# Optimization experiments

Measured on AMD Instinct MI355X. Metric: run time of the kernel, lower is better.

Reference implementation:

```python
import jax, jax.numpy as jnp
import numpy as np

B = 8192
NV = 778   # MANO vertices
NJ = 16    # LBS joints
PARENTS = np.array([0, 0, 1, 2, 0, 4, 5, 0, 7, 8, 0, 10, 11, 0, 13, 14])


def quat2mat(quat):
    # quat: [N,4] (w,x,y,z) -> [N,3,3]
    q = quat / jnp.linalg.norm(quat, axis=1, keepdims=True)
    w, x, y, z = q[:, 0], q[:, 1], q[:, 2], q[:, 3]
    w2, x2, y2, z2 = w * w, x * x, y * y, z * z
    wx, wy, wz = w * x, w * y, w * z
    xy, xz, yz = x * y, x * z, y * z
    R = jnp.stack([
        w2 + x2 - y2 - z2, 2 * xy - 2 * wz, 2 * wy + 2 * xz,
        2 * wz + 2 * xy, w2 - x2 + y2 - z2, 2 * yz - 2 * wx,
        2 * xz - 2 * wy, 2 * wx + 2 * yz, w2 - x2 - y2 + z2,
    ], axis=1)
    return R.reshape(-1, 3, 3)


def batch_rodrigues(theta):
    # theta: [N,3] axis-angle -> [N,3,3]
    angle = jnp.linalg.norm(theta + 1e-8, axis=1, keepdims=True)
    normalized = theta / angle
    half = angle * 0.5
    quat = jnp.concatenate([jnp.cos(half), jnp.sin(half) * normalized], axis=1)
    return quat2mat(quat)


def qmul(q, r):
    # Hamilton product, (w,x,y,z); q,r: [N,4]
    w1, x1, y1, z1 = q[:, 0], q[:, 1], q[:, 2], q[:, 3]
    w2, x2, y2, z2 = r[:, 0], r[:, 1], r[:, 2], r[:, 3]
    return jnp.stack([
        w1 * w2 - x1 * x2 - y1 * y2 - z1 * z2,
        w1 * x2 + x1 * w2 + y1 * z2 - z1 * y2,
        w1 * y2 - x1 * z2 + y1 * w2 + z1 * x2,
        w1 * z2 + x1 * y2 - y1 * x2 + z1 * w2,
    ], axis=1)


def make_A(R, t):
    # R: [B,J,3,3], t: [B,J,3] -> [B,J,4,4]
    Bn, J = R.shape[0], R.shape[1]
    top = jnp.concatenate([R, t[..., None]], axis=-1)              # [B,J,3,4]
    bot = jnp.broadcast_to(jnp.array([0., 0., 0., 1.], R.dtype), (Bn, J, 1, 4))
    return jnp.concatenate([top, bot], axis=-2)


def mano_forward(theta, delta_quat, user_shape, init_quat, init_trans,
                 v_template, shapedirs, J_regressor, posedirs, weights):
    Bn = theta.shape[0]
    beta = jnp.broadcast_to(user_shape, (Bn, user_shape.shape[-1]))
    v_shaped = (beta @ shapedirs).reshape(Bn, NV, 3) + v_template   # [B,778,3]
    J = jnp.einsum('bvc,vj->bjc', v_shaped, J_regressor)            # [B,21,3]

    Rs = batch_rodrigues(theta.reshape(-1, 3)).reshape(Bn, 15, 3, 3)
    pose_feature = (Rs - jnp.eye(3, dtype=Rs.dtype)).reshape(Bn, 135)
    v_posed = (pose_feature @ posedirs).reshape(Bn, NV, 3) + v_shaped

    quat = qmul(delta_quat, jnp.broadcast_to(init_quat, (Bn, 4)))
    root_R = quat2mat(quat)                                          # [B,3,3]
    Rs_all = jnp.concatenate([root_R[:, None], Rs], axis=1)          # [B,16,3,3]

    Jk = J[:, :NJ]                                                   # [B,16,3]
    rel = Jk - Jk[:, PARENTS]
    rel = rel.at[:, 0].set(Jk[:, 0])                                 # root keeps absolute pos
    A_local = make_A(Rs_all, rel)                                    # [B,16,4,4]

    # kinematic chain (fixed 16-joint tree)
    results = [A_local[:, 0]]
    for i in range(1, NJ):
        results.append(results[PARENTS[i]] @ A_local[:, i])
    G = jnp.stack(results, axis=1)                                   # [B,16,4,4]

    Jw0 = jnp.concatenate([Jk, jnp.zeros((Bn, NJ, 1), Jk.dtype)], axis=-1)
    init_bone = jnp.einsum('bjkl,bjl->bjk', G, Jw0)                  # [B,16,4]
    A = jnp.concatenate([G[..., :3], G[..., 3:] - init_bone[..., None]], axis=-1)

    T = jnp.einsum('vj,bjkl->bvkl', weights, A)                      # [B,778,4,4]
    vp_homo = jnp.concatenate([v_posed, jnp.ones((Bn, NV, 1), v_posed.dtype)], axis=-1)
    verts = jnp.einsum('bvkl,bvl->bvk', T, vp_homo)[..., :3]         # [B,778,3]

    joints = jnp.einsum('bvc,vj->bjc', verts, J_regressor)           # [B,21,3]
    trans = init_trans.reshape(Bn, 1, 3)
    return joints + trans  # get_skin=False path


def setup_inputs() -> dict:
    key = jax.random.key(0)
    ks = jax.random.split(key, 10)
    return {
        'theta': jax.random.normal(ks[0], (B, 45), jnp.float32) * 0.3,
        'delta_quat': jax.random.normal(ks[1], (B, 4), jnp.float32),
        'user_shape': jax.random.normal(ks[2], (1, 10), jnp.float32),
        'init_quat': jax.random.normal(ks[3], (1, 4), jnp.float32),
        'init_trans': jax.random.normal(ks[4], (B, 3), jnp.float32),
        'v_template': jax.random.normal(ks[5], (NV, 3), jnp.float32),
        'shapedirs': jax.random.normal(ks[6], (10, NV * 3), jnp.float32) * 0.01,
        'J_regressor': jax.random.uniform(ks[7], (NV, 21), jnp.float32) / NV,
        'posedirs': jax.random.normal(ks[8], (135, NV * 3), jnp.float32) * 0.01,
        'weights': jax.random.uniform(ks[9], (NV, NJ), jnp.float32),
    }


def reference(theta, delta_quat, user_shape, init_quat, init_trans,
              v_template, shapedirs, J_regressor, posedirs, weights):
    return mano_forward(theta, delta_quat, user_shape, init_quat, init_trans,
                        v_template, shapedirs, J_regressor, posedirs, weights)
```

## Files before the change

kernel.cpp:

```cpp
#include <hip/hip_runtime.h>
#include <math.h>

#define B_SIZE 8192
#define NVERT 778
#define NP 135
#define NEC 416
#define KS16 16

#define OFF_JK    0
#define OFF_C1    64
#define OFF_C0    400
#define OFF_P2    1408
#define OFF_PFT   137488
#define OFF_AT    1243408
#define OFF_PP    137488
#define WS_END    2816272

__device__ inline void quat2mat_dev(float qw, float qx, float qy, float qz, float* R) {
  float n = sqrtf(qw*qw + qx*qx + qy*qy + qz*qz);
  float w = qw/n, x = qx/n, y = qy/n, z = qz/n;
  float w2=w*w, x2=x*x, y2=y*y, z2=z*z;
  float wx=w*x, wy=w*y, wz=w*z, xy=x*y, xz=x*z, yz=y*z;
  R[0]=w2+x2-y2-z2; R[1]=2.f*xy-2.f*wz; R[2]=2.f*wy+2.f*xz;
  R[3]=2.f*wz+2.f*xy; R[4]=w2-x2+y2-z2; R[5]=2.f*yz-2.f*wx;
  R[6]=2.f*xz-2.f*wy; R[7]=2.f*wx+2.f*yz; R[8]=w2-x2-y2+z2;
}

__device__ inline void rodrigues_dev(float tx, float ty, float tz, float* R) {
  float ax = tx + 1e-8f, ay = ty + 1e-8f, az = tz + 1e-8f;
  float angle = sqrtf(ax*ax + ay*ay + az*az);
  float nx = tx/angle, ny = ty/angle, nz = tz/angle;
  float half = 0.5f*angle;
  float cw = cosf(half), sw = sinf(half);
  quat2mat_dev(cw, sw*nx, sw*ny, sw*nz, R);
}

__global__ __launch_bounds__(256) void kA(const float* __restrict__ J_regressor,
                                          const float* __restrict__ weights,
                                          const float* __restrict__ posedirs,
                                          const float* __restrict__ user_shape,
                                          const float* __restrict__ v_template,
                                          const float* __restrict__ shapedirs,
                                          float* __restrict__ ws) {
  int tid = threadIdx.x;
  int bid = blockIdx.x;

  if (bid >= 416) {
    int j = bid - 416;
    __shared__ float red[3*256];
    __shared__ float ush[10];
    if (tid < 10) ush[tid] = user_shape[tid];
    __syncthreads();
    float p0 = 0.f, p1 = 0.f, p2 = 0.f;
    for (int v = tid; v < NVERT; v += 256) {
      float jr = J_regressor[v*21 + j];
      #pragma unroll
      for (int c = 0; c < 3; ++c) {
        int e = 3*v + c;
        float t = v_template[e];
        #pragma unroll
        for (int s = 0; s < 10; ++s) t += ush[s]*shapedirs[s*2334 + e];
        float val = jr * t;
        if (c == 0) p0 += val; else if (c == 1) p1 += val; else p2 += val;
      }
    }
    red[0*256+tid] = p0; red[1*256+tid] = p1; red[2*256+tid] = p2;
    __syncthreads();
    for (int s = 128; s > 0; s >>= 1) {
      if (tid < s) {
        red[0*256+tid] += red[0*256+tid+s];
        red[1*256+tid] += red[1*256+tid+s];
        red[2*256+tid] += red[2*256+tid+s];
      }
      __syncthreads();
    }
    if (tid < 3) ws[OFF_JK + j*3 + tid] = red[tid*256];
    return;
  }

  __shared__ float sJR[49*21];
  __shared__ float sW [49*16];
  __shared__ float sB [64*16];
  __shared__ float ush[10];
  if (tid < 10) ush[tid] = user_shape[tid];
  int ng = bid % 26;
  int ks = bid / 26;
  int vbeg = ks*49;
  int kt = min(NVERT - vbeg, 49);
  __syncthreads();
  for (int idx = tid; idx < kt*21; idx += 256) sJR[idx] = J_regressor[vbeg*21 + idx];
  for (int idx = tid; idx < kt*16; idx += 256) sW[idx]  = weights[vbeg*16 + idx];
  for (int idx = tid; idx < 16*64; idx += 256) {
    int s = idx >> 6, iv = idx & 63;
    if (iv < kt) {
      int ec = ng*16 + s;
      float val;
      if (ec > 408) val = 0.f;
      else if (ec == 408) val = 1.f;
      else {
        int c = ec / 136, pp = ec - c*136;
        int e = 3*(vbeg+iv) + c;
        if (pp == 135) {
          float t = v_template[e];
          #pragma unroll
          for (int s0 = 0; s0 < 10; ++s0) t += ush[s0]*shapedirs[s0*2334 + e];
          val = t;
        } else {
          val = posedirs[pp*2334 + e];
        }
      }
      sB[iv*16 + s] = val;
    }
  }
  __syncthreads();
  if (tid < 168) {
    int cg2 = (tid < 84) ? 0 : 1;
    int r4  = (tid < 84) ? tid : tid - 84;
    int q2 = 4*r4;
    int j2 = q2 >> 4;
    int jb = q2 & 15;
    float acc[4][8];
    #pragma unroll
    for (int r = 0; r < 4; ++r)
      #pragma unroll
      for (int s = 0; s < 8; ++s) acc[r][s] = 0.f;
    for (int i = 0; i < kt; ++i) {
      float jr = sJR[i*21 + j2];
      float4 w4 = *(const float4*)&sW[i*16 + jb];
      float4 b0 = *(const float4*)&sB[i*16 + cg2*8];
      float4 b1 = *(const float4*)&sB[i*16 + cg2*8 + 4];
      float wv[4] = {w4.x, w4.y, w4.z, w4.w};
      #pragma unroll
      for (int r = 0; r < 4; ++r) {
        float s2 = jr * wv[r];
        acc[r][0] += s2*b0.x; acc[r][1] += s2*b0.y;
        acc[r][2] += s2*b0.z; acc[r][3] += s2*b0.w;
        acc[r][4] += s2*b1.x; acc[r][5] += s2*b1.y;
        acc[r][6] += s2*b1.z; acc[r][7] += s2*b1.w;
      }
    }
    float* Pp = ws + OFF_PP + (size_t)ks*NEC*336;
    #pragma unroll
    for (int s = 0; s < 8; ++s) {
      int ec = ng*16 + cg2*8 + s;
      float4 v4 = make_float4(acc[0][s], acc[1][s], acc[2][s], acc[3][s]);
      *(float4*)&Pp[ec*336 + q2] = v4;
    }
  }
}

__global__ void kR(float* __restrict__ ws) {
  int idx = blockIdx.x*256 + threadIdx.x;
  if (idx >= 416*84) return;
  int ec = idx / 84, q4 = idx - ec*84;
  const float* Pp = ws + OFF_PP;
  float4 s = make_float4(0.f, 0.f, 0.f, 0.f);
  #pragma unroll
  for (int ks = 0; ks < KS16; ++ks) {
    float4 v = *(const float4*)&Pp[(size_t)ks*NEC*336 + ec*336 + 4*q4];
    s.x += v.x; s.y += v.y; s.z += v.z; s.w += v.w;
  }
  float sv[4] = {s.x, s.y, s.z, s.w};
  #pragma unroll
  for (int r = 0; r < 4; ++r) {
    int q2 = 4*q4 + r;
    int jj2 = q2 >> 4, jj = q2 & 15;
    if (ec < 408) {
      int c = ec / 136, pp = ec - c*136;
      if (pp < 135) ws[OFF_P2 + (size_t)(jj2*135 + pp)*48 + jj*3 + c] = sv[r];
      else          ws[OFF_C0 + jj2*48 + jj*3 + c] = sv[r];
    } else if (ec == 408) {
      ws[OFF_C1 + jj2*16 + jj] = sv[r];
    }
  }
}

__global__ __launch_bounds__(256) void k4_pose(const float* __restrict__ theta,
                                               const float* __restrict__ delta_quat,
                                               const float* __restrict__ init_quat,
                                               float* __restrict__ ws) {
  int bid = blockIdx.x;
  int u  = bid % 6;
  int bb = bid / 6;
  int b  = bb*256 + threadIdx.x;
  __shared__ float jk[48], rel[48];
  if (threadIdx.x < 48) {
    float v = ws[OFF_JK + threadIdx.x];
    jk[threadIdx.x] = v;
    int j = threadIdx.x/3, c = threadIdx.x - j*3;
    float r;
    if (j == 0) r = v;
    else {
      int par = (((j-1) % 3) == 0) ? 0 : (j-1);
      r = v - ws[OFF_JK + par*3 + c];
    }
    rel[threadIdx.x] = r;
  }
  __syncthreads();
  float* pfT = ws + OFF_PFT;
  float* AT  = ws + OFF_AT;

  float w1=delta_quat[b*4+0], x1=delta_quat[b*4+1], y1=delta_quat[b*4+2], z1=delta_quat[b*4+3];
  float w2=init_quat[0], x2=init_quat[1], y2=init_quat[2], z2=init_quat[3];
  float qw = w1*w2 - x1*x2 - y1*y2 - z1*z2;
  float qx = w1*x2 + x1*w2 + y1*z2 - z1*y2;
  float qy = w1*y2 - x1*z2 + y1*w2 + z1*x2;
  float qz = w1*z2 + x1*y2 - y1*x2 + z1*w2;
  float G[12];
  quat2mat_dev(qw, qx, qy, qz, G);
  G[9] = rel[0]; G[10] = rel[1]; G[11] = rel[2];

  if (u == 5) {
    #pragma unroll
    for (int c = 0; c < 3; ++c) {
      float g0 = G[c*3+0], g1 = G[c*3+1], g2 = G[c*3+2];
      AT[(size_t)(c*4+0)*B_SIZE + b] = g0;
      AT[(size_t)(c*4+1)*B_SIZE + b] = g1;
      AT[(size_t)(c*4+2)*B_SIZE + b] = g2;
      AT[(size_t)(c*4+3)*B_SIZE + b] = G[9+c] - (g0*jk[0] + g1*jk[1] + g2*jk[2]);
    }
    return;
  }

  #pragma unroll
  for (int mstep = 0; mstep < 3; ++mstep) {
    int j = 3*u + 1 + mstep;
    int i = j - 1;
    float R[9];
    rodrigues_dev(theta[b*45+3*i+0], theta[b*45+3*i+1], theta[b*45+3*i+2], R);
    pfT[(size_t)(9*i+0)*B_SIZE + b] = R[0]-1.f;
    pfT[(size_t)(9*i+1)*B_SIZE + b] = R[1];
    pfT[(size_t)(9*i+2)*B_SIZE + b] = R[2];
    pfT[(size_t)(9*i+3)*B_SIZE + b] = R[3];
    pfT[(size_t)(9*i+4)*B_SIZE + b] = R[4]-1.f;
    pfT[(size_t)(9*i+5)*B_SIZE + b] = R[5];
    pfT[(size_t)(9*i+6)*B_SIZE + b] = R[6];
    pfT[(size_t)(9*i+7)*B_SIZE + b] = R[7];
    pfT[(size_t)(9*i+8)*B_SIZE + b] = R[8]-1.f;
    float nG[12];
    const float* rj = rel + j*3;
    #pragma unroll
    for (int r3 = 0; r3 < 3; ++r3) {
      float a0 = G[r3*3+0], a1 = G[r3*3+1], a2 = G[r3*3+2];
      nG[r3*3+0] = a0*R[0] + a1*R[3] + a2*R[6];
      nG[r3*3+1] = a0*R[1] + a1*R[4] + a2*R[7];
      nG[r3*3+2] = a0*R[2] + a1*R[5] + a2*R[8];
      nG[9+r3]   = G[9+r3] + a0*rj[0] + a1*rj[1] + a2*rj[2];
    }
    #pragma unroll
    for (int k = 0; k < 12; ++k) G[k] = nG[k];
    const float* jkj = jk + j*3;
    #pragma unroll
    for (int c = 0; c < 3; ++c) {
      float g0 = G[c*3+0], g1 = G[c*3+1], g2 = G[c*3+2];
      AT[(size_t)(j*12 + c*4+0)*B_SIZE + b] = g0;
      AT[(size_t)(j*12 + c*4+1)*B_SIZE + b] = g1;
      AT[(size_t)(j*12 + c*4+2)*B_SIZE + b] = g2;
      AT[(size_t)(j*12 + c*4+3)*B_SIZE + b] = G[9+c] - (g0*jkj[0] + g1*jkj[1] + g2*jkj[2]);
    }
  }
}

__global__ __launch_bounds__(256) void k5_main(const float* __restrict__ init_trans,
                                               const float* __restrict__ ws,
                                               float* __restrict__ out) {
  int g = blockIdx.x;
  int xcd = g & 7, k = g >> 3;
  int br  = ((k & 3) << 3) | xcd;
  int j2  = k >> 2;
  int b   = br*256 + threadIdx.x;

  float4 acc[12];
  const float4* c04 = (const float4*)(ws + OFF_C0 + j2*48);
  #pragma unroll
  for (int i = 0; i < 12; ++i) acc[i] = c04[i];

  const float* pfT = ws + OFF_PFT;
  const float4* P24 = (const float4*)(ws + OFF_P2);
  #pragma unroll 3
  for (int p = 0; p < NP; ++p) {
    float pf = pfT[(size_t)p*B_SIZE + b];
    const float4* Pr = P24 + (size_t)(j2*135 + p)*12;
    #pragma unroll
    for (int i = 0; i < 12; ++i) {
      float4 pv = Pr[i];
      acc[i].x += pf*pv.x; acc[i].y += pf*pv.y;
      acc[i].z += pf*pv.z; acc[i].w += pf*pv.w;
    }
  }

  float m[48];
  #pragma unroll
  for (int i = 0; i < 12; ++i) {
    m[4*i+0] = acc[i].x; m[4*i+1] = acc[i].y;
    m[4*i+2] = acc[i].z; m[4*i+3] = acc[i].w;
  }

  const float* AT  = ws + OFF_AT;
  const float* c1p = ws + OFF_C1 + j2*16;
  float o0 = 0.f, o1 = 0.f, o2 = 0.f;
  #pragma unroll
  for (int j = 0; j < 16; ++j) {
    float c1 = c1p[j];
    float m0 = m[3*j+0], m1 = m[3*j+1], m2 = m[3*j+2];
    #pragma unroll
    for (int k2 = 0; k2 < 3; ++k2) {
      float a0 = AT[(size_t)(j*12 + k2*4+0)*B_SIZE + b];
      float a1 = AT[(size_t)(j*12 + k2*4+1)*B_SIZE + b];
      float a2 = AT[(size_t)(j*12 + k2*4+2)*B_SIZE + b];
      float a3 = AT[(size_t)(j*12 + k2*4+3)*B_SIZE + b];
      float r = a0*m0 + a1*m1 + a2*m2 + a3*c1;
      if (k2 == 0) o0 += r; else if (k2 == 1) o1 += r; else o2 += r;
    }
  }
  size_t ob = ((size_t)b*21 + j2)*3;
  out[ob+0] = o0 + init_trans[b*3+0];
  out[ob+1] = o1 + init_trans[b*3+1];
  out[ob+2] = o2 + init_trans[b*3+2];
}

extern "C" void kernel_launch(void* const* d_in, const int* in_sizes, int n_in,
                              void* d_out, int out_size, void* d_ws, size_t ws_size,
                              hipStream_t stream) {
  const float* theta       = (const float*)d_in[0];
  const float* delta_quat  = (const float*)d_in[1];
  const float* user_shape  = (const float*)d_in[2];
  const float* init_quat   = (const float*)d_in[3];
  const float* init_trans  = (const float*)d_in[4];
  const float* v_template  = (const float*)d_in[5];
  const float* shapedirs   = (const float*)d_in[6];
  const float* J_regressor = (const float*)d_in[7];
  const float* posedirs    = (const float*)d_in[8];
  const float* weights     = (const float*)d_in[9];
  float* out = (float*)d_out;
  float* ws  = (float*)d_ws;

  kA<<<432, 256, 0, stream>>>(J_regressor, weights, posedirs,
                              user_shape, v_template, shapedirs, ws);
  kR<<<137, 256, 0, stream>>>(ws);
  k4_pose<<<192, 256, 0, stream>>>(theta, delta_quat, init_quat, ws);
  k5_main<<<672, 256, 0, stream>>>(init_trans, ws, out);
}
```

Before: 142.9 us.

## Merge reduce and pose kernels, split k5 pose-blendshape loop across two waves

Moves the partial-sum buffer to a non-overlapping workspace region so the reduction and pose kernels can run as one launch, removing one launch and its serialization. A fallback path keeps the old three-kernel sequence when the workspace is too small. k5_main now uses 512 threads per block: each half handles half of the 135 pose features, and the two partial accumulators are combined through shared memory. This doubles the parallelism of the posedirs GEMV at the cost of about 49 KB of LDS per block, which can limit occupancy. Pose blocks are also remapped so consecutive blocks fall on different XCDs.

Measured after the change: 193.2 us. +35.2%, slower.

```diff
diff --git a/kernel.cpp b/kernel.cpp
--- a/kernel.cpp
+++ b/kernel.cpp
@@ -13,8 +13,9 @@
 #define OFF_P2    1408
 #define OFF_PFT   137488
 #define OFF_AT    1243408
-#define OFF_PP    137488
-#define WS_END    2816272
+#define WS_BASE   2816272
+#define OFF_PP_OVER 137488
+#define OFF_PP_SAFE 2816272
 
 __device__ inline void quat2mat_dev(float qw, float qx, float qy, float qz, float* R) {
   float n = sqrtf(qw*qw + qx*qx + qy*qy + qz*qz);
@@ -35,13 +36,106 @@
   quat2mat_dev(cw, sw*nx, sw*ny, sw*nz, R);
 }
 
+__device__ inline void pose_unit(const float* __restrict__ theta,
+                                 const float* __restrict__ delta_quat,
+                                 const float* __restrict__ init_quat,
+                                 float* __restrict__ ws,
+                                 const float* jk, const float* rel,
+                                 int bb, int u, int lane) {
+  int b = bb*256 + lane;
+  float* pfT = ws + OFF_PFT;
+  float* AT  = ws + OFF_AT;
+  float w1=delta_quat[b*4+0], x1=delta_quat[b*4+1], y1=delta_quat[b*4+2], z1=delta_quat[b*4+3];
+  float w2=init_quat[0], x2=init_quat[1], y2=init_quat[2], z2=init_quat[3];
+  float qw = w1*w2 - x1*x2 - y1*y2 - z1*z2;
+  float qx = w1*x2 + x1*w2 + y1*z2 - z1*y2;
+  float qy = w1*y2 - x1*z2 + y1*w2 + z1*x2;
+  float qz = w1*z2 + x1*y2 - y1*x2 + z1*w2;
+  float G[12];
+  quat2mat_dev(qw, qx, qy, qz, G);
+  G[9] = rel[0]; G[10] = rel[1]; G[11] = rel[2];
+  if (u == 5) {
+    #pragma unroll
+    for (int c = 0; c < 3; ++c) {
+      float g0 = G[c*3+0], g1 = G[c*3+1], g2 = G[c*3+2];
+      AT[(size_t)(c*4+0)*B_SIZE + b] = g0;
+      AT[(size_t)(c*4+1)*B_SIZE + b] = g1;
+      AT[(size_t)(c*4+2)*B_SIZE + b] = g2;
+      AT[(size_t)(c*4+3)*B_SIZE + b] = G[9+c] - (g0*jk[0] + g1*jk[1] + g2*jk[2]);
+    }
+    return;
+  }
+  #pragma unroll
+  for (int mstep = 0; mstep < 3; ++mstep) {
+    int j = 3*u + 1 + mstep;
+    int i = j - 1;
+    float R[9];
+    rodrigues_dev(theta[b*45+3*i+0], theta[b*45+3*i+1], theta[b*45+3*i+2], R);
+    pfT[(size_t)(9*i+0)*B_SIZE + b] = R[0]-1.f;
+    pfT[(size_t)(9*i+1)*B_SIZE + b] = R[1];
+    pfT[(size_t)(9*i+2)*B_SIZE + b] = R[2];
+    pfT[(size_t)(9*i+3)*B_SIZE + b] = R[3];
+    pfT[(size_t)(9*i+4)*B_SIZE + b] = R[4]-1.f;
+    pfT[(size_t)(9*i+5)*B_SIZE + b] = R[5];
+    pfT[(size_t)(9*i+6)*B_SIZE + b] = R[6];
+    pfT[(size_t)(9*i+7)*B_SIZE + b] = R[7];
+    pfT[(size_t)(9*i+8)*B_SIZE + b] = R[8]-1.f;
+    float nG[12];
+    const float* rj = rel + j*3;
+    #pragma unroll
+    for (int r3 = 0; r3 < 3; ++r3) {
+      float a0 = G[r3*3+0], a1 = G[r3*3+1], a2 = G[r3*3+2];
+      nG[r3*3+0] = a0*R[0] + a1*R[3] + a2*R[6];
+      nG[r3*3+1] = a0*R[1] + a1*R[4] + a2*R[7];
+      nG[r3*3+2] = a0*R[2] + a1*R[5] + a2*R[8];
+      nG[9+r3]   = G[9+r3] + a0*rj[0] + a1*rj[1] + a2*rj[2];
+    }
+    #pragma unroll
+    for (int k = 0; k < 12; ++k) G[k] = nG[k];
+    const float* jkj = jk + j*3;
+    #pragma unroll
+    for (int c = 0; c < 3; ++c) {
+      float g0 = G[c*3+0], g1 = G[c*3+1], g2 = G[c*3+2];
+      AT[(size_t)(j*12 + c*4+0)*B_SIZE + b] = g0;
+      AT[(size_t)(j*12 + c*4+1)*B_SIZE + b] = g1;
+      AT[(size_t)(j*12 + c*4+2)*B_SIZE + b] = g2;
+      AT[(size_t)(j*12 + c*4+3)*B_SIZE + b] = G[9+c] - (g0*jkj[0] + g1*jkj[1] + g2*jkj[2]);
+    }
+  }
+}
+
+__device__ inline void kr_task(float* __restrict__ ws, int pp_off, int idx) {
+  if (idx >= 416*84) return;
+  int ec = idx / 84, q4 = idx - ec*84;
+  const float* Pp = ws + pp_off;
+  float4 s = make_float4(0.f, 0.f, 0.f, 0.f);
+  #pragma unroll
+  for (int ks = 0; ks < KS16; ++ks) {
+    float4 v = *(const float4*)&Pp[(size_t)ks*NEC*336 + ec*336 + 4*q4];
+    s.x += v.x; s.y += v.y; s.z += v.z; s.w += v.w;
+  }
+  float sv[4] = {s.x, s.y, s.z, s.w};
+  #pragma unroll
+  for (int r = 0; r < 4; ++r) {
+    int q2 = 4*q4 + r;
+    int jj2 = q2 >> 4, jj = q2 & 15;
+    if (ec < 408) {
+      int c = ec / 136, pp = ec - c*136;
+      if (pp < 135) ws[OFF_P2 + (size_t)(jj2*135 + pp)*48 + jj*3 + c] = sv[r];
+      else          ws[OFF_C0 + jj2*48 + jj*3 + c] = sv[r];
+    } else if (ec == 408) {
+      ws[OFF_C1 + jj2*16 + jj] = sv[r];
+    }
+  }
+}
+
 __global__ __launch_bounds__(256) void kA(const float* __restrict__ J_regressor,
                                           const float* __restrict__ weights,
                                           const float* __restrict__ posedirs,
                                           const float* __restrict__ user_shape,
                                           const float* __restrict__ v_template,
                                           const float* __restrict__ shapedirs,
-                                          float* __restrict__ ws) {
+                                          float* __restrict__ ws, int pp_off) {
   int tid = threadIdx.x;
   int bid = blockIdx.x;
 
@@ -139,7 +233,7 @@
         acc[r][6] += s2*b1.z; acc[r][7] += s2*b1.w;
       }
     }
-    float* Pp = ws + OFF_PP + (size_t)ks*NEC*336;
+    float* Pp = ws + pp_off + (size_t)ks*NEC*336;
     #pragma unroll
     for (int s = 0; s < 8; ++s) {
       int ec = ng*16 + cg2*8 + s;
@@ -149,138 +243,100 @@
   }
 }
 
-__global__ void kR(float* __restrict__ ws) {
-  int idx = blockIdx.x*256 + threadIdx.x;
-  if (idx >= 416*84) return;
-  int ec = idx / 84, q4 = idx - ec*84;
-  const float* Pp = ws + OFF_PP;
-  float4 s = make_float4(0.f, 0.f, 0.f, 0.f);
-  #pragma unroll
-  for (int ks = 0; ks < KS16; ++ks) {
-    float4 v = *(const float4*)&Pp[(size_t)ks*NEC*336 + ec*336 + 4*q4];
-    s.x += v.x; s.y += v.y; s.z += v.z; s.w += v.w;
-  }
-  float sv[4] = {s.x, s.y, s.z, s.w};
-  #pragma unroll
-  for (int r = 0; r < 4; ++r) {
-    int q2 = 4*q4 + r;
-    int jj2 = q2 >> 4, jj = q2 & 15;
-    if (ec < 408) {
-      int c = ec / 136, pp = ec - c*136;
-      if (pp < 135) ws[OFF_P2 + (size_t)(jj2*135 + pp)*48 + jj*3 + c] = sv[r];
-      else          ws[OFF_C0 + jj2*48 + jj*3 + c] = sv[r];
-    } else if (ec == 408) {
-      ws[OFF_C1 + jj2*16 + jj] = sv[r];
-    }
-  }
-}
-
-__global__ __launch_bounds__(256) void k4_pose(const float* __restrict__ theta,
-                                               const float* __restrict__ delta_quat,
-                                               const float* __restrict__ init_quat,
-                                               float* __restrict__ ws) {
+__global__ __launch_bounds__(256) void kRk4(const float* __restrict__ theta,
+                                            const float* __restrict__ delta_quat,
+                                            const float* __restrict__ init_quat,
+                                            float* __restrict__ ws, int pp_off) {
   int bid = blockIdx.x;
-  int u  = bid % 6;
-  int bb = bid / 6;
-  int b  = bb*256 + threadIdx.x;
+  int tid = threadIdx.x;
+  if (bid < 137) {
+    kr_task(ws, pp_off, bid*256 + tid);
+    return;
+  }
   __shared__ float jk[48], rel[48];
-  if (threadIdx.x < 48) {
-    float v = ws[OFF_JK + threadIdx.x];
-    jk[threadIdx.x] = v;
-    int j = threadIdx.x/3, c = threadIdx.x - j*3;
+  if (tid < 48) {
+    float v = ws[OFF_JK + tid];
+    jk[tid] = v;
+    int j = tid/3, c = tid - j*3;
     float r;
     if (j == 0) r = v;
     else {
       int par = (((j-1) % 3) == 0) ? 0 : (j-1);
       r = v - ws[OFF_JK + par*3 + c];
     }
-    rel[threadIdx.x] = r;
+    rel[tid] = r;
   }
   __syncthreads();
-  float* pfT = ws + OFF_PFT;
-  float* AT  = ws + OFF_AT;
-
-  float w1=delta_quat[b*4+0], x1=delta_quat[b*4+1], y1=delta_quat[b*4+2], z1=delta_quat[b*4+3];
-  float w2=init_quat[0], x2=init_quat[1], y2=init_quat[2], z2=init_quat[3];
-  float qw = w1*w2 - x1*x2 - y1*y2 - z1*z2;
-  float qx = w1*x2 + x1*w2 + y1*z2 - z1*y2;
-  float qy = w1*y2 - x1*z2 + y1*w2 + z1*x2;
-  float qz = w1*z2 + x1*y2 - y1*x2 + z1*w2;
-  float G[12];
-  quat2mat_dev(qw, qx, qy, qz, G);
-  G[9] = rel[0]; G[10] = rel[1]; G[11] = rel[2];
-
-  if (u == 5) {
-    #pragma unroll
-    for (int c = 0; c < 3; ++c) {
-      float g0 = G[c*3+0], g1 = G[c*3+1], g2 = G[c*3+2];
-      AT[(size_t)(c*4+0)*B_SIZE + b] = g0;
-      AT[(size_t)(c*4+1)*B_SIZE + b] = g1;
-      AT[(size_t)(c*4+2)*B_SIZE + b] = g2;
-      AT[(size_t)(c*4+3)*B_SIZE + b] = G[9+c] - (g0*jk[0] + g1*jk[1] + g2*jk[2]);
-    }
-    return;
-  }
-
-  #pragma unroll
-  for (int mstep = 0; mstep < 3; ++mstep) {
-    int j = 3*u + 1 + mstep;
-    int i = j - 1;
-    float R[9];
-    rodrigues_dev(theta[b*45+3*i+0], theta[b*45+3*i+1], theta[b*45+3*i+2], R);
-    pfT[(size_t)(9*i+0)*B_SIZE + b] = R[0]-1.f;
-    pfT[(size_t)(9*i+1)*B_SIZE + b] = R[1];
-    pfT[(size_t)(9*i+2)*B_SIZE + b] = R[2];
-    pfT[(size_t)(9*i+3)*B_SIZE + b] = R[3];
-    pfT[(size_t)(9*i+4)*B_SIZE + b] = R[4]-1.f;
-    pfT[(size_t)(9*i+5)*B_SIZE + b] = R[5];
-    pfT[(size_t)(9*i+6)*B_SIZE + b] = R[6];
-    pfT[(size_t)(9*i+7)*B_SIZE + b] = R[7];
-    pfT[(size_t)(9*i+8)*B_SIZE + b] = R[8]-1.f;
-    float nG[12];
-    const float* rj = rel + j*3;
-    #pragma unroll
-    for (int r3 = 0; r3 < 3; ++r3) {
-      float a0 = G[r3*3+0], a1 = G[r3*3+1], a2 = G[r3*3+2];
-      nG[r3*3+0] = a0*R[0] + a1*R[3] + a2*R[6];
-      nG[r3*3+1] = a0*R[1] + a1*R[4] + a2*R[7];
-      nG[r3*3+2] = a0*R[2] + a1*R[5] + a2*R[8];
-      nG[9+r3]   = G[9+r3] + a0*rj[0] + a1*rj[1] + a2*rj[2];
-    }
-    #pragma unroll
-    for (int k = 0; k < 12; ++k) G[k] = nG[k];
-    const float* jkj = jk + j*3;
-    #pragma unroll
-    for (int c = 0; c < 3; ++c) {
-      float g0 = G[c*3+0], g1 = G[c*3+1], g2 = G[c*3+2];
-      AT[(size_t)(j*12 + c*4+0)*B_SIZE + b] = g0;
-      AT[(size_t)(j*12 + c*4+1)*B_SIZE + b] = g1;
-      AT[(size_t)(j*12 + c*4+2)*B_SIZE + b] = g2;
-      AT[(size_t)(j*12 + c*4+3)*B_SIZE + b] = G[9+c] - (g0*jkj[0] + g1*jkj[1] + g2*jkj[2]);
-    }
-  }
-}
-
-__global__ __launch_bounds__(256) void k5_main(const float* __restrict__ init_trans,
+  int s = bid & 7;
+  int t = (bid - 137) >> 3;
+  int bb = s + 8*(t & 3);
+  int u  = t >> 2;
+  pose_unit(theta, delta_quat, init_quat, ws, jk, rel, bb, u, tid);
+}
+
+__global__ void kR_fb(float* __restrict__ ws, int pp_off) {
+  kr_task(ws, pp_off, blockIdx.x*256 + threadIdx.x);
+}
+
+__global__ __launch_bounds__(256) void k4_fb(const float* __restrict__ theta,
+                                             const float* __restrict__ delta_quat,
+                                             const float* __restrict__ init_quat,
+                                             float* __restrict__ ws) {
+  int bid = blockIdx.x;
+  int tid = threadIdx.x;
+  __shared__ float jk[48], rel[48];
+  if (tid < 48) {
+    float v = ws[OFF_JK + tid];
+    jk[tid] = v;
+    int j = tid/3, c = tid - j*3;
+    float r;
+    if (j == 0) r = v;
+    else {
+      int par = (((j-1) % 3) == 0) ? 0 : (j-1);
+      r = v - ws[OFF_JK + par*3 + c];
+    }
+    rel[tid] = r;
+  }
+  __syncthreads();
+  int s = bid & 7;
+  int t = bid >> 3;
+  int bb = s + 8*(t & 3);
+  int u  = t >> 2;
+  pose_unit(theta, delta_quat, init_quat, ws, jk, rel, bb, u, tid);
+}
+
+__global__ __launch_bounds__(512) void k5_main(const float* __restrict__ init_trans,
                                                const float* __restrict__ ws,
                                                float* __restrict__ out) {
+  __shared__ float sM[256*49];
   int g = blockIdx.x;
   int xcd = g & 7, k = g >> 3;
   int br  = ((k & 3) << 3) | xcd;
   int j2  = k >> 2;
-  int b   = br*256 + threadIdx.x;
+  int tid = threadIdx.x;
+  int bl  = tid & 255;
+  int ph  = tid >> 8;
+  int b   = br*256 + bl;
+
+  int pbeg = __builtin_amdgcn_readfirstlane(ph ? 68 : 0);
+  int pend = __builtin_amdgcn_readfirstlane(ph ? NP : 68);
 
   float4 acc[12];
-  const float4* c04 = (const float4*)(ws + OFF_C0 + j2*48);
-  #pragma unroll
-  for (int i = 0; i < 12; ++i) acc[i] = c04[i];
+  if (ph == 0) {
+    const float4* c04 = (const float4*)(ws + OFF_C0 + j2*48);
+    #pragma unroll
+    for (int i = 0; i < 12; ++i) acc[i] = c04[i];
+  } else {
+    #pragma unroll
+    for (int i = 0; i < 12; ++i) acc[i] = make_float4(0.f, 0.f, 0.f, 0.f);
+  }
 
   const float* pfT = ws + OFF_PFT;
-  const float4* P24 = (const float4*)(ws + OFF_P2);
+  const float4* P24 = (const float4*)(ws + OFF_P2) + (size_t)j2*1620;
   #pragma unroll 3
-  for (int p = 0; p < NP; ++p) {
+  for (int p = pbeg; p < pend; ++p) {
     float pf = pfT[(size_t)p*B_SIZE + b];
-    const float4* Pr = P24 + (size_t)(j2*135 + p)*12;
+    const float4* Pr = P24 + p*12;
     #pragma unroll
     for (int i = 0; i < 12; ++i) {
       float4 pv = Pr[i];
@@ -289,34 +345,47 @@
     }
   }
 
-  float m[48];
-  #pragma unroll
-  for (int i = 0; i < 12; ++i) {
-    m[4*i+0] = acc[i].x; m[4*i+1] = acc[i].y;
-    m[4*i+2] = acc[i].z; m[4*i+3] = acc[i].w;
-  }
-
-  const float* AT  = ws + OFF_AT;
-  const float* c1p = ws + OFF_C1 + j2*16;
-  float o0 = 0.f, o1 = 0.f, o2 = 0.f;
-  #pragma unroll
-  for (int j = 0; j < 16; ++j) {
-    float c1 = c1p[j];
-    float m0 = m[3*j+0], m1 = m[3*j+1], m2 = m[3*j+2];
-    #pragma unroll
-    for (int k2 = 0; k2 < 3; ++k2) {
-      float a0 = AT[(size_t)(j*12 + k2*4+0)*B_SIZE + b];
-      float a1 = AT[(size_t)(j*12 + k2*4+1)*B_SIZE + b];
-      float a2 = AT[(size_t)(j*12 + k2*4+2)*B_SIZE + b];
-      float a3 = AT[(size_t)(j*12 + k2*4+3)*B_SIZE + b];
-      float r = a0*m0 + a1*m1 + a2*m2 + a3*c1;
-      if (k2 == 0) o0 += r; else if (k2 == 1) o1 += r; else o2 += r;
-    }
-  }
-  size_t ob = ((size_t)b*21 + j2)*3;
-  out[ob+0] = o0 + init_trans[b*3+0];
-  out[ob+1] = o1 + init_trans[b*3+1];
-  out[ob+2] = o2 + init_trans[b*3+2];
+  if (ph == 1) {
+    float* dst = sM + bl*49;
+    #pragma unroll
+    for (int i = 0; i < 12; ++i) {
+      dst[4*i+0] = acc[i].x; dst[4*i+1] = acc[i].y;
+      dst[4*i+2] = acc[i].z; dst[4*i+3] = acc[i].w;
+    }
+  }
+  __syncthreads();
+  if (ph == 0) {
+    const float* src = sM + bl*49;
+    float m[48];
+    #pragma unroll
+    for (int i = 0; i < 12; ++i) {
+      m[4*i+0] = acc[i].x + src[4*i+0];
+      m[4*i+1] = acc[i].y + src[4*i+1];
+      m[4*i+2] = acc[i].z + src[4*i+2];
+      m[4*i+3] = acc[i].w + src[4*i+3];
+    }
+    const float* AT  = ws + OFF_AT;
+    const float* c1p = ws + OFF_C1 + j2*16;
+    float o0 = 0.f, o1 = 0.f, o2 = 0.f;
+    #pragma unroll
+    for (int j = 0; j < 16; ++j) {
+      float c1 = c1p[j];
+      float m0 = m[3*j+0], m1 = m[3*j+1], m2 = m[3*j+2];
+      #pragma unroll
+      for (int k2 = 0; k2 < 3; ++k2) {
+        float a0 = AT[(size_t)(j*12 + k2*4+0)*B_SIZE + b];
+        float a1 = AT[(size_t)(j*12 + k2*4+1)*B_SIZE + b];
+        float a2 = AT[(size_t)(j*12 + k2*4+2)*B_SIZE + b];
+        float a3 = AT[(size_t)(j*12 + k2*4+3)*B_SIZE + b];
+        float r = a0*m0 + a1*m1 + a2*m2 + a3*c1;
+        if (k2 == 0) o0 += r; else if (k2 == 1) o1 += r; else o2 += r;
+      }
+    }
+    size_t ob = ((size_t)b*21 + j2)*3;
+    out[ob+0] = o0 + init_trans[b*3+0];
+    out[ob+1] = o1 + init_trans[b*3+1];
+    out[ob+2] = o2 + init_trans[b*3+2];
+  }
 }
 
 extern "C" void kernel_launch(void* const* d_in, const int* in_sizes, int n_in,
@@ -335,9 +404,16 @@
   float* out = (float*)d_out;
   float* ws  = (float*)d_ws;
 
-  kA<<<432, 256, 0, stream>>>(J_regressor, weights, posedirs,
-                              user_shape, v_template, shapedirs, ws);
-  kR<<<137, 256, 0, stream>>>(ws);
-  k4_pose<<<192, 256, 0, stream>>>(theta, delta_quat, init_quat, ws);
-  k5_main<<<672, 256, 0, stream>>>(init_trans, ws, out);
-}
+  size_t need = ((size_t)OFF_PP_SAFE + (size_t)KS16*NEC*336) * 4;
+  if (ws_size >= need) {
+    kA<<<432, 256, 0, stream>>>(J_regressor, weights, posedirs,
+                                user_shape, v_template, shapedirs, ws, OFF_PP_SAFE);
+    kRk4<<<329, 256, 0, stream>>>(theta, delta_quat, init_quat, ws, OFF_PP_SAFE);
+  } else {
+    kA<<<432, 256, 0, stream>>>(J_regressor, weights, posedirs,
+                                user_shape, v_template, shapedirs, ws, OFF_PP_OVER);
+    kR_fb<<<137, 256, 0, stream>>>(ws, OFF_PP_OVER);
+    k4_fb<<<192, 256, 0, stream>>>(theta, delta_quat, init_quat, ws);
+  }
+  k5_main<<<672, 512, 0, stream>>>(init_trans, ws, out);
+}
```

## Fuse precompute, reduction and pose kernels into a single prep kernel

Applied to the files above, without the earlier changes.

Replaces the three preparatory kernels (split-K weight contraction, partial-sum reduction, pose chain) with one kernel. The weight contraction now runs one block per output row over the full vertex range, so the split-K partial buffer and the separate reduction pass are gone. The pose blocks each recompute the joint locations locally with a wave-shuffle reduction instead of reading them from a prior kernel. This removes two launches and the workspace round trip, at the cost of redundant joint-regression work in every pose block and less parallel, scalar-FMA contraction per block.

Measured after the change: 183.8 us. 1.29x slower.

```diff
diff --git a/kernel.cpp b/kernel.cpp
--- a/kernel.cpp
+++ b/kernel.cpp
@@ -4,8 +4,6 @@
 #define B_SIZE 8192
 #define NVERT 778
 #define NP 135
-#define NEC 416
-#define KS16 16
 
 #define OFF_JK    0
 #define OFF_C1    64
@@ -13,7 +11,6 @@
 #define OFF_P2    1408
 #define OFF_PFT   137488
 #define OFF_AT    1243408
-#define OFF_PP    137488
 #define WS_END    2816272
 
 __device__ inline void quat2mat_dev(float qw, float qx, float qy, float qz, float* R) {
@@ -35,171 +32,15 @@
   quat2mat_dev(cw, sw*nx, sw*ny, sw*nz, R);
 }
 
-__global__ __launch_bounds__(256) void kA(const float* __restrict__ J_regressor,
-                                          const float* __restrict__ weights,
-                                          const float* __restrict__ posedirs,
-                                          const float* __restrict__ user_shape,
-                                          const float* __restrict__ v_template,
-                                          const float* __restrict__ shapedirs,
-                                          float* __restrict__ ws) {
-  int tid = threadIdx.x;
-  int bid = blockIdx.x;
-
-  if (bid >= 416) {
-    int j = bid - 416;
-    __shared__ float red[3*256];
-    __shared__ float ush[10];
-    if (tid < 10) ush[tid] = user_shape[tid];
-    __syncthreads();
-    float p0 = 0.f, p1 = 0.f, p2 = 0.f;
-    for (int v = tid; v < NVERT; v += 256) {
-      float jr = J_regressor[v*21 + j];
-      #pragma unroll
-      for (int c = 0; c < 3; ++c) {
-        int e = 3*v + c;
-        float t = v_template[e];
-        #pragma unroll
-        for (int s = 0; s < 10; ++s) t += ush[s]*shapedirs[s*2334 + e];
-        float val = jr * t;
-        if (c == 0) p0 += val; else if (c == 1) p1 += val; else p2 += val;
-      }
-    }
-    red[0*256+tid] = p0; red[1*256+tid] = p1; red[2*256+tid] = p2;
-    __syncthreads();
-    for (int s = 128; s > 0; s >>= 1) {
-      if (tid < s) {
-        red[0*256+tid] += red[0*256+tid+s];
-        red[1*256+tid] += red[1*256+tid+s];
-        red[2*256+tid] += red[2*256+tid+s];
-      }
-      __syncthreads();
-    }
-    if (tid < 3) ws[OFF_JK + j*3 + tid] = red[tid*256];
-    return;
-  }
-
-  __shared__ float sJR[49*21];
-  __shared__ float sW [49*16];
-  __shared__ float sB [64*16];
-  __shared__ float ush[10];
-  if (tid < 10) ush[tid] = user_shape[tid];
-  int ng = bid % 26;
-  int ks = bid / 26;
-  int vbeg = ks*49;
-  int kt = min(NVERT - vbeg, 49);
-  __syncthreads();
-  for (int idx = tid; idx < kt*21; idx += 256) sJR[idx] = J_regressor[vbeg*21 + idx];
-  for (int idx = tid; idx < kt*16; idx += 256) sW[idx]  = weights[vbeg*16 + idx];
-  for (int idx = tid; idx < 16*64; idx += 256) {
-    int s = idx >> 6, iv = idx & 63;
-    if (iv < kt) {
-      int ec = ng*16 + s;
-      float val;
-      if (ec > 408) val = 0.f;
-      else if (ec == 408) val = 1.f;
-      else {
-        int c = ec / 136, pp = ec - c*136;
-        int e = 3*(vbeg+iv) + c;
-        if (pp == 135) {
-          float t = v_template[e];
-          #pragma unroll
-          for (int s0 = 0; s0 < 10; ++s0) t += ush[s0]*shapedirs[s0*2334 + e];
-          val = t;
-        } else {
-          val = posedirs[pp*2334 + e];
-        }
-      }
-      sB[iv*16 + s] = val;
-    }
-  }
-  __syncthreads();
-  if (tid < 168) {
-    int cg2 = (tid < 84) ? 0 : 1;
-    int r4  = (tid < 84) ? tid : tid - 84;
-    int q2 = 4*r4;
-    int j2 = q2 >> 4;
-    int jb = q2 & 15;
-    float acc[4][8];
-    #pragma unroll
-    for (int r = 0; r < 4; ++r)
-      #pragma unroll
-      for (int s = 0; s < 8; ++s) acc[r][s] = 0.f;
-    for (int i = 0; i < kt; ++i) {
-      float jr = sJR[i*21 + j2];
-      float4 w4 = *(const float4*)&sW[i*16 + jb];
-      float4 b0 = *(const float4*)&sB[i*16 + cg2*8];
-      float4 b1 = *(const float4*)&sB[i*16 + cg2*8 + 4];
-      float wv[4] = {w4.x, w4.y, w4.z, w4.w};
-      #pragma unroll
-      for (int r = 0; r < 4; ++r) {
-        float s2 = jr * wv[r];
-        acc[r][0] += s2*b0.x; acc[r][1] += s2*b0.y;
-        acc[r][2] += s2*b0.z; acc[r][3] += s2*b0.w;
-        acc[r][4] += s2*b1.x; acc[r][5] += s2*b1.y;
-        acc[r][6] += s2*b1.z; acc[r][7] += s2*b1.w;
-      }
-    }
-    float* Pp = ws + OFF_PP + (size_t)ks*NEC*336;
-    #pragma unroll
-    for (int s = 0; s < 8; ++s) {
-      int ec = ng*16 + cg2*8 + s;
-      float4 v4 = make_float4(acc[0][s], acc[1][s], acc[2][s], acc[3][s]);
-      *(float4*)&Pp[ec*336 + q2] = v4;
-    }
-  }
-}
-
-__global__ void kR(float* __restrict__ ws) {
-  int idx = blockIdx.x*256 + threadIdx.x;
-  if (idx >= 416*84) return;
-  int ec = idx / 84, q4 = idx - ec*84;
-  const float* Pp = ws + OFF_PP;
-  float4 s = make_float4(0.f, 0.f, 0.f, 0.f);
-  #pragma unroll
-  for (int ks = 0; ks < KS16; ++ks) {
-    float4 v = *(const float4*)&Pp[(size_t)ks*NEC*336 + ec*336 + 4*q4];
-    s.x += v.x; s.y += v.y; s.z += v.z; s.w += v.w;
-  }
-  float sv[4] = {s.x, s.y, s.z, s.w};
-  #pragma unroll
-  for (int r = 0; r < 4; ++r) {
-    int q2 = 4*q4 + r;
-    int jj2 = q2 >> 4, jj = q2 & 15;
-    if (ec < 408) {
-      int c = ec / 136, pp = ec - c*136;
-      if (pp < 135) ws[OFF_P2 + (size_t)(jj2*135 + pp)*48 + jj*3 + c] = sv[r];
-      else          ws[OFF_C0 + jj2*48 + jj*3 + c] = sv[r];
-    } else if (ec == 408) {
-      ws[OFF_C1 + jj2*16 + jj] = sv[r];
-    }
-  }
-}
-
-__global__ __launch_bounds__(256) void k4_pose(const float* __restrict__ theta,
-                                               const float* __restrict__ delta_quat,
-                                               const float* __restrict__ init_quat,
-                                               float* __restrict__ ws) {
-  int bid = blockIdx.x;
-  int u  = bid % 6;
-  int bb = bid / 6;
-  int b  = bb*256 + threadIdx.x;
-  __shared__ float jk[48], rel[48];
-  if (threadIdx.x < 48) {
-    float v = ws[OFF_JK + threadIdx.x];
-    jk[threadIdx.x] = v;
-    int j = threadIdx.x/3, c = threadIdx.x - j*3;
-    float r;
-    if (j == 0) r = v;
-    else {
-      int par = (((j-1) % 3) == 0) ? 0 : (j-1);
-      r = v - ws[OFF_JK + par*3 + c];
-    }
-    rel[threadIdx.x] = r;
-  }
-  __syncthreads();
+__device__ inline void pose_unit(const float* __restrict__ theta,
+                                 const float* __restrict__ delta_quat,
+                                 const float* __restrict__ init_quat,
+                                 float* __restrict__ ws,
+                                 const float* jk, const float* rel,
+                                 int bb, int u, int lane) {
+  int b = bb*256 + lane;
   float* pfT = ws + OFF_PFT;
   float* AT  = ws + OFF_AT;
-
   float w1=delta_quat[b*4+0], x1=delta_quat[b*4+1], y1=delta_quat[b*4+2], z1=delta_quat[b*4+3];
   float w2=init_quat[0], x2=init_quat[1], y2=init_quat[2], z2=init_quat[3];
   float qw = w1*w2 - x1*x2 - y1*y2 - z1*z2;
@@ -209,7 +50,6 @@
   float G[12];
   quat2mat_dev(qw, qx, qy, qz, G);
   G[9] = rel[0]; G[10] = rel[1]; G[11] = rel[2];
-
   if (u == 5) {
     #pragma unroll
     for (int c = 0; c < 3; ++c) {
@@ -221,7 +61,6 @@
     }
     return;
   }
-
   #pragma unroll
   for (int mstep = 0; mstep < 3; ++mstep) {
     int j = 3*u + 1 + mstep;
@@ -261,6 +100,137 @@
   }
 }
 
+__global__ __launch_bounds__(384) void kPrep(const float* __restrict__ theta,
+                                             const float* __restrict__ delta_quat,
+                                             const float* __restrict__ init_quat,
+                                             const float* __restrict__ v_template,
+                                             const float* __restrict__ user_shape,
+                                             const float* __restrict__ shapedirs,
+                                             const float* __restrict__ J_regressor,
+                                             const float* __restrict__ posedirs,
+                                             const float* __restrict__ weights,
+                                             float* __restrict__ ws) {
+  __shared__ float smem[4928];
+  int tid = threadIdx.x;
+  int bid = blockIdx.x;
+
+  if (bid < 409) {
+    float* sJR = smem;
+    float* sW  = smem + 2688;
+    float* sB  = smem + 4736;
+    float* ush = smem + 4864;
+    if (tid < 10) ush[tid] = user_shape[tid];
+    int ec = bid;
+    int cc = ec / 136, pp = ec - cc*136;
+    int q2 = tid;
+    int j2 = q2 >> 4, jj = q2 & 15;
+    float acc = 0.f;
+    for (int v0 = 0; v0 < NVERT; v0 += 128) {
+      int kt = min(128, NVERT - v0);
+      __syncthreads();
+      for (int i = tid; i < kt*21; i += 384) sJR[i] = J_regressor[v0*21 + i];
+      for (int i = tid; i < kt*16; i += 384) sW[i]  = weights[v0*16 + i];
+      for (int i = tid; i < kt; i += 384) {
+        float val;
+        if (ec == 408) val = 1.f;
+        else {
+          int e = 3*(v0+i) + cc;
+          if (pp == 135) {
+            float t = v_template[e];
+            #pragma unroll
+            for (int s = 0; s < 10; ++s) t += ush[s]*shapedirs[s*2334 + e];
+            val = t;
+          } else {
+            val = posedirs[pp*2334 + e];
+          }
+        }
+        sB[i] = val;
+      }
+      __syncthreads();
+      if (tid < 336) {
+        for (int i = 0; i < kt; ++i) {
+          float bv = sB[i];
+          acc += sJR[i*21 + j2] * sW[i*16 + jj] * bv;
+        }
+      }
+    }
+    if (tid < 336) {
+      if (ec == 408) {
+        ws[OFF_C1 + j2*16 + jj] = acc;
+      } else if (pp == 135) {
+        ws[OFF_C0 + j2*48 + jj*3 + cc] = acc;
+      } else {
+        ws[OFF_P2 + (size_t)(j2*135 + pp)*48 + jj*3 + cc] = acc;
+      }
+    }
+    return;
+  }
+
+  float* redw = smem;
+  float* jk   = smem + 288;
+  float* rel  = smem + 336;
+  float* ush  = smem + 384;
+  if (tid < 10) ush[tid] = user_shape[tid];
+  __syncthreads();
+  float part[48];
+  #pragma unroll
+  for (int k = 0; k < 48; ++k) part[k] = 0.f;
+  for (int v = tid; v < NVERT; v += 384) {
+    float vs[3];
+    #pragma unroll
+    for (int c = 0; c < 3; ++c) {
+      int e = 3*v + c;
+      float t = v_template[e];
+      #pragma unroll
+      for (int s = 0; s < 10; ++s) t += ush[s]*shapedirs[s*2334 + e];
+      vs[c] = t;
+    }
+    #pragma unroll
+    for (int j = 0; j < 16; ++j) {
+      float jr = J_regressor[v*21 + j];
+      part[j*3+0] += jr*vs[0];
+      part[j*3+1] += jr*vs[1];
+      part[j*3+2] += jr*vs[2];
+    }
+  }
+  int lane = tid & 63, wid = tid >> 6;
+  #pragma unroll
+  for (int k = 0; k < 48; ++k) {
+    float v = part[k];
+    v += __shfl_down(v, 32);
+    v += __shfl_down(v, 16);
+    v += __shfl_down(v, 8);
+    v += __shfl_down(v, 4);
+    v += __shfl_down(v, 2);
+    v += __shfl_down(v, 1);
+    if (lane == 0) redw[wid*48 + k] = v;
+  }
+  __syncthreads();
+  if (tid < 48) {
+    float s = 0.f;
+    #pragma unroll
+    for (int w = 0; w < 6; ++w) s += redw[w*48 + tid];
+    jk[tid] = s;
+  }
+  __syncthreads();
+  if (tid < 48) {
+    int j = tid/3, c = tid - j*3;
+    float r;
+    if (j == 0) r = jk[tid];
+    else {
+      int par = (((j-1) % 3) == 0) ? 0 : (j-1);
+      r = jk[tid] - jk[par*3 + c];
+    }
+    rel[tid] = r;
+  }
+  __syncthreads();
+  if (tid < 256) {
+    int pid = bid - 409;
+    int bb = pid / 6, u = pid - 6*bb;
+    pose_unit(theta, delta_quat, init_quat, ws, jk, rel, bb, u, tid);
+  }
+}
+
 __global__ __launch_bounds__(256) void k5_main(const float* __restrict__ init_trans,
                                                const float* __restrict__ ws,
                                                float* __restrict__ out) {
@@ -335,9 +305,8 @@
   float* out = (float*)d_out;
   float* ws  = (float*)d_ws;
 
-  kA<<<432, 256, 0, stream>>>(J_regressor, weights, posedirs,
-                              user_shape, v_template, shapedirs, ws);
-  kR<<<137, 256, 0, stream>>>(ws);
-  k4_pose<<<192, 256, 0, stream>>>(theta, delta_quat, init_quat, ws);
+  kPrep<<<601, 384, 0, stream>>>(theta, delta_quat, init_quat, v_template,
+                                 user_shape, shapedirs, J_regressor, posedirs,
+                                 weights, ws);
   k5_main<<<672, 256, 0, stream>>>(init_trans, ws, out);
 }
```
